# Kernel tuning notes

Hardware: AMD Instinct MI355X
Metric: run time of the kernel (lower is better)

## Reference

```python
import jax, jax.numpy as jnp
import numpy as np

NEG = -1000000.0

def setup_inputs() -> dict:
    key = jax.random.key(0)
    k1, k2, k3, k4 = jax.random.split(key, 4)
    B, S, D = 32, 2048, 64  # batch_eff=batch*heads, seq_len, head_dim
    queries = jax.random.normal(k1, (B, S, D), dtype=jnp.float32)
    keys = jax.random.normal(k2, (B, S, D), dtype=jnp.float32)
    values = jax.random.normal(k3, (B, S, D), dtype=jnp.float32)
    valid_len = jax.random.randint(k4, (B,), 1, S + 1, dtype=jnp.int32)
    return {"queries": queries, "keys": keys, "values": values, "valid_len": valid_len}

def reference(queries, keys, values, valid_len):
    # scores: (B, Sq, Sk) = QK^T / sqrt(d)
    d = queries.shape[-1]
    scores = jnp.einsum('bqd,bkd->bqk', queries, keys) / jnp.sqrt(jnp.float32(d))
    # padding mask from per-batch valid key lengths: True where position is padded
    k_len = keys.shape[1]
    pad_mask = jnp.arange(k_len)[None, None, :] >= valid_len[:, None, None]  # (B,1,Sk)
    scores = jnp.where(pad_mask, NEG, scores)
    attn = jax.nn.softmax(scores, axis=-1)
    # dropout is identity in eval / reference mode
    return jnp.einsum('bqk,bkd->bqd', attn, values)
```

## Files before the change

### kernel.cpp

```cpp
#include <hip/hip_runtime.h>

typedef unsigned short ushort_t;
typedef short short8 __attribute__((ext_vector_type(8)));
typedef float f32x4 __attribute__((ext_vector_type(4)));
typedef unsigned int u32x4 __attribute__((ext_vector_type(4)));

typedef f32x4 f32x4a __attribute__((may_alias));
typedef u32x4 u32x4a __attribute__((may_alias));
typedef short8 short8a __attribute__((may_alias));

#define BC 64
#define PRP 74

#define BAR_LGKM() asm volatile("s_waitcnt lgkmcnt(0)\n\ts_barrier" ::: "memory")
#define BAR_VM4()  asm volatile("s_waitcnt vmcnt(4)\n\ts_barrier" ::: "memory")
#define BAR_VM0()  asm volatile("s_waitcnt vmcnt(0)\n\ts_barrier" ::: "memory")

__device__ __forceinline__ ushort_t f2bf(float x) {
    unsigned u = __float_as_uint(x);
    u = (u + 0x7fffu + ((u >> 16) & 1u)) >> 16;
    return (ushort_t)u;
}

__device__ __forceinline__ void dma16(const void* g, void* lds) {
    __builtin_amdgcn_global_load_lds(
        (const __attribute__((address_space(1))) unsigned int*)g,
        (__attribute__((address_space(3))) unsigned int*)lds, 16, 0, 0);
}

__global__ __launch_bounds__(256) void prep_kv(
    const float* __restrict__ K, const float* __restrict__ V,
    ushort_t* __restrict__ Kb, ushort_t* __restrict__ Vt, int S, int jtiles)
{
    __shared__ ushort_t T[64 * 66];
    const int b  = blockIdx.x / jtiles;
    const int j0 = (blockIdx.x % jtiles) * 64;
    const int tid = threadIdx.x;

    {
        const int jj = tid >> 2, d0 = (tid & 3) * 16;
        const float* src = K + ((size_t)b * S + j0 + jj) * 64 + d0;
        f32x4 k0 = *(const f32x4a*)(src),     k1 = *(const f32x4a*)(src + 4);
        f32x4 k2 = *(const f32x4a*)(src + 8), k3 = *(const f32x4a*)(src + 12);
        u32x4 w0, w1;
#pragma unroll
        for (int k = 0; k < 2; ++k) {
            w0[k]   = (unsigned)f2bf(k0[2*k]) | ((unsigned)f2bf(k0[2*k+1]) << 16);
            w0[k+2] = (unsigned)f2bf(k1[2*k]) | ((unsigned)f2bf(k1[2*k+1]) << 16);
            w1[k]   = (unsigned)f2bf(k2[2*k]) | ((unsigned)f2bf(k2[2*k+1]) << 16);
            w1[k+2] = (unsigned)f2bf(k3[2*k]) | ((unsigned)f2bf(k3[2*k+1]) << 16);
        }
        ushort_t* dst = Kb + ((size_t)b * S + j0 + jj) * 64 + d0;
        *(u32x4a*)dst = w0;
        *(u32x4a*)(dst + 8) = w1;
    }

    {
        const float* Vb = V + ((size_t)b * S + j0) * 64;
#pragma unroll
        for (int p = 0; p < 4; ++p) {
            int jj = p * 16 + (tid >> 4), d4 = (tid & 15) * 4;
            f32x4 v = *(const f32x4a*)(Vb + (size_t)jj * 64 + d4);
#pragma unroll
            for (int k = 0; k < 4; ++k) T[(d4 + k) * 66 + jj] = f2bf(v[k]);
        }
        __syncthreads();
        const int d = tid >> 2, j16 = (tid & 3) * 16;
        ushort_t* dst = Vt + ((size_t)b * 64 + d) * S + j0 + j16;
        u32x4 w0, w1;
#pragma unroll
        for (int k = 0; k < 4; ++k) {
            w0[k] = (unsigned)T[d*66 + j16 + 2*k]     | ((unsigned)T[d*66 + j16 + 2*k + 1] << 16);
            w1[k] = (unsigned)T[d*66 + j16 + 8 + 2*k] | ((unsigned)T[d*66 + j16 + 9 + 2*k] << 16);
        }
        *(u32x4a*)dst = w0;
        *(u32x4a*)(dst + 8) = w1;
    }
}

__global__ __launch_bounds__(256, 3) void attn_persist(
    const float* __restrict__ Q, const ushort_t* __restrict__ Kb,
    const ushort_t* __restrict__ Vt, const int* __restrict__ VL,
    float* __restrict__ O, int* __restrict__ cnt,
    int NB, int S, int qtiles, int nitems)
{
    __shared__ __align__(16) ushort_t Kbuf[2][64 * 64];
    __shared__ __align__(16) ushort_t Vbuf[2][64 * 64];
    __shared__ ushort_t Psh[4 * 16 * PRP];
    __shared__ int order_s[64];
    __shared__ int item_s;

    const int tid  = threadIdx.x;
    const int wave = tid >> 6;
    const int lane = tid & 63;
    const int qd   = lane >> 4;
    const int c    = lane & 15;
    const int q8   = qd * 8;

    if (tid < NB && NB <= 64) {
        const int myL = VL[tid];
        int rank = 0;
        for (int j = 0; j < NB; ++j) {
            const int Lj = VL[j];
            rank += (Lj > myL) || (Lj == myL && j < tid);
        }
        order_s[rank] = tid;
    }
    __syncthreads();

    const int r0 = 8 * (wave * 2) + (lane >> 3);
    const int r1 = r0 + 8;
    const int bdp = lane & 7;
    const int swz0 = ((bdp - r0) & 7) * 16;
    const int swz1 = ((bdp - r1) & 7) * 16;
    const int ldsoff0 = (wave * 2) * 512;
    const int ldsoff1 = ldsoff0 + 512;

    int off[2][4];
#pragma unroll
    for (int x = 0; x < 2; ++x)
#pragma unroll
        for (int y = 0; y < 4; ++y) {
            const int row = y * 16 + c;
            off[x][y] = row * 128 + (((x * 4 + qd) + row) & 7) * 16;
        }

    const float qs = 0.125f * 1.4426950408889634f;
    const f32x4 zero4 = {0.0f, 0.0f, 0.0f, 0.0f};
    ushort_t* Pw = Psh + wave * (16 * PRP);

    for (;;) {
        if (tid == 0) item_s = atomicAdd(cnt, 1);
        __syncthreads();
        const int it = item_s;
        if (it >= nitems) break;

        const int b  = order_s[it / qtiles];
        const int qt = it % qtiles;
        const int qrow0 = qt * 64 + wave * 16;
        const int L   = VL[b];
        const int nkt = (L + BC - 1) / BC;

        short8 qf[2];
        {
            const float* Qb = Q + ((size_t)b * S + qrow0) * 64;
#pragma unroll
            for (int kc = 0; kc < 2; ++kc) {
                const float* p = Qb + c * 64 + kc * 32 + q8;
                f32x4 a = *(const f32x4a*)p;
                f32x4 bq = *(const f32x4a*)(p + 4);
                short8 f;
#pragma unroll
                for (int k = 0; k < 4; ++k) {
                    f[k]   = (short)f2bf(a[k] * qs);
                    f[k+4] = (short)f2bf(bq[k] * qs);
                }
                qf[kc] = f;
            }
        }

        f32x4 oacc[4];
#pragma unroll
        for (int dt = 0; dt < 4; ++dt) oacc[dt] = zero4;
        float lrow[4] = {0.0f, 0.0f, 0.0f, 0.0f};

        const char* KbB = (const char*)(Kb + (size_t)b * S * 64);
        const char* VtB = (const char*)(Vt + (size_t)b * 64 * S);
        const char* kg0 = KbB + r0 * 128 + swz0;
        const char* kg1 = KbB + r1 * 128 + swz1;
        const char* vg0 = VtB + (size_t)r0 * (S * 2) + swz0;
        const char* vg1 = VtB + (size_t)r1 * (S * 2) + swz1;

        dma16(kg0, Kbuf[0] + ldsoff0);
        dma16(kg1, Kbuf[0] + ldsoff1);
        dma16(vg0, Vbuf[0] + ldsoff0);
        dma16(vg1, Vbuf[0] + ldsoff1);

        for (int kt = 0; kt < nkt; ++kt) {
            const int j0 = kt * BC;
            const ushort_t* Kt  = Kbuf[kt & 1];
            const ushort_t* Vb_ = Vbuf[kt & 1];

            if (kt + 1 < nkt) {
                const size_t ko = (size_t)(kt + 1) * 8192;
                const size_t vo = (size_t)(kt + 1) * 128;
                ushort_t* kb = Kbuf[(kt + 1) & 1];
                ushort_t* vb = Vbuf[(kt + 1) & 1];
                dma16(kg0 + ko, kb + ldsoff0);
                dma16(kg1 + ko, kb + ldsoff1);
                dma16(vg0 + vo, vb + ldsoff0);
                dma16(vg1 + vo, vb + ldsoff1);
                BAR_VM4();
            } else {
                BAR_VM0();
            }

            f32x4 sacc[4];
#pragma unroll
            for (int nt = 0; nt < 4; ++nt) sacc[nt] = zero4;
#pragma unroll
            for (int kc = 0; kc < 2; ++kc) {
#pragma unroll
                for (int nt = 0; nt < 4; ++nt) {
                    short8 kf = *(const short8a*)((const char*)Kt + off[kc][nt]);
                    sacc[nt] = __builtin_amdgcn_mfma_f32_16x16x32_bf16(qf[kc], kf, sacc[nt], 0, 0, 0);
                }
            }

#pragma unroll
            for (int nt = 0; nt < 4; ++nt) {
                const bool valid = (j0 + nt * 16 + c) < L;
#pragma unroll
                for (int r = 0; r < 4; ++r) {
                    float p = valid ? exp2f(sacc[nt][r]) : 0.0f;
                    lrow[r] += p;
                    Pw[(qd * 4 + r) * PRP + nt * 16 + c] = f2bf(p);
                }
            }

#pragma unroll
            for (int jc = 0; jc < 2; ++jc) {
                short8 pf = *(const short8a*)&Pw[c * PRP + jc * 32 + q8];
#pragma unroll
                for (int dt = 0; dt < 4; ++dt) {
                    short8 vf = *(const short8a*)((const char*)Vb_ + off[jc][dt]);
                    oacc[dt] = __builtin_amdgcn_mfma_f32_16x16x32_bf16(pf, vf, oacc[dt], 0, 0, 0);
                }
            }

            BAR_LGKM();
        }

#pragma unroll
        for (int r = 0; r < 4; ++r) {
            float ls = lrow[r];
            ls += __shfl_xor(ls, 1);
            ls += __shfl_xor(ls, 2);
            ls += __shfl_xor(ls, 4);
            ls += __shfl_xor(ls, 8);
            const float inv = 1.0f / ls;
            const int row = qrow0 + qd * 4 + r;
            float* dst = O + ((size_t)b * S + row) * 64;
#pragma unroll
            for (int dt = 0; dt < 4; ++dt)
                dst[dt * 16 + c] = oacc[dt][r] * inv;
        }
    }
}

__global__ __launch_bounds__(256, 4) void attn_mono(
    const float* __restrict__ Q, const float* __restrict__ K,
    const float* __restrict__ V, const int* __restrict__ VL,
    float* __restrict__ O, int NB, int S)
{
    __shared__ ushort_t Ksh[BC * PRP];
    __shared__ ushort_t Vsh[64 * PRP];
    __shared__ ushort_t Psh[4 * 16 * PRP];
    const int tid = threadIdx.x, wave = tid >> 6, lane = tid & 63;
    const int qd = lane >> 4, c = lane & 15, q8 = qd * 8;
    const int bid = blockIdx.x;
    const int b = (bid & 7) | (((bid >> 3) & 3) << 3);
    const int qt = bid >> 5;
    const int qrow0 = qt * 64 + wave * 16;
    const int L = VL[b];
    const int nkt = (L + BC - 1) / BC;
    const size_t bbase = (size_t)b * S * 64;
    const int kj = tid >> 2, kd = (tid & 3) * 16;
    const int vp = tid & 31, vd = (tid >> 5) * 8;
    const float qs = 0.125f * 1.4426950408889634f;
    short8 qf[2];
    {
        const float* Qb = Q + bbase + (size_t)qrow0 * 64;
#pragma unroll
        for (int kc = 0; kc < 2; ++kc) {
            const float* p = Qb + c * 64 + kc * 32 + q8;
            f32x4 a = *(const f32x4a*)p;
            f32x4 bq = *(const f32x4a*)(p + 4);
            short8 f;
#pragma unroll
            for (int k = 0; k < 4; ++k) { f[k] = (short)f2bf(a[k]*qs); f[k+4] = (short)f2bf(bq[k]*qs); }
            qf[kc] = f;
        }
    }
    const f32x4 zero4 = {0.0f, 0.0f, 0.0f, 0.0f};
    f32x4 oacc[4];
#pragma unroll
    for (int dt = 0; dt < 4; ++dt) oacc[dt] = zero4;
    float lrow[4] = {0, 0, 0, 0};
    ushort_t* Pw = Psh + wave * (16 * PRP);
    for (int kt = 0; kt < nkt; ++kt) {
        const int j0 = kt * BC;
        __syncthreads();
        {
            const float* src = K + bbase + (size_t)(j0 + kj) * 64 + kd;
            f32x4 k0 = *(const f32x4a*)(src), k1 = *(const f32x4a*)(src + 4);
            f32x4 k2 = *(const f32x4a*)(src + 8), k3 = *(const f32x4a*)(src + 12);
            u32x4 w0, w1;
#pragma unroll
            for (int k = 0; k < 2; ++k) {
                w0[k]   = (unsigned)f2bf(k0[2*k]) | ((unsigned)f2bf(k0[2*k+1]) << 16);
                w0[k+2] = (unsigned)f2bf(k1[2*k]) | ((unsigned)f2bf(k1[2*k+1]) << 16);
                w1[k]   = (unsigned)f2bf(k2[2*k]) | ((unsigned)f2bf(k2[2*k+1]) << 16);
                w1[k+2] = (unsigned)f2bf(k3[2*k]) | ((unsigned)f2bf(k3[2*k+1]) << 16);
            }
            *(u32x4a*)&Ksh[kj * PRP + kd] = w0;
            *(u32x4a*)&Ksh[kj * PRP + kd + 8] = w1;
        }
        {
            const float* src = V + bbase + (size_t)(j0 + 2 * vp) * 64 + vd;
            f32x4 a0 = *(const f32x4a*)(src), a1 = *(const f32x4a*)(src + 4);
            f32x4 b0 = *(const f32x4a*)(src + 64), b1 = *(const f32x4a*)(src + 68);
#pragma unroll
            for (int kk = 0; kk < 8; ++kk) {
                float av = (kk < 4) ? a0[kk & 3] : a1[kk & 3];
                float bv = (kk < 4) ? b0[kk & 3] : b1[kk & 3];
                *(unsigned __attribute__((may_alias))*)&Vsh[(vd + kk) * PRP + 2 * vp] =
                    (unsigned)f2bf(av) | ((unsigned)f2bf(bv) << 16);
            }
        }
        __syncthreads();
        f32x4 sacc[4];
#pragma unroll
        for (int nt = 0; nt < 4; ++nt) sacc[nt] = zero4;
#pragma unroll
        for (int kc = 0; kc < 2; ++kc)
#pragma unroll
            for (int nt = 0; nt < 4; ++nt) {
                short8 kf = *(const short8a*)&Ksh[(nt * 16 + c) * PRP + kc * 32 + q8];
                sacc[nt] = __builtin_amdgcn_mfma_f32_16x16x32_bf16(qf[kc], kf, sacc[nt], 0, 0, 0);
            }
#pragma unroll
        for (int nt = 0; nt < 4; ++nt) {
            const bool valid = (j0 + nt * 16 + c) < L;
#pragma unroll
            for (int r = 0; r < 4; ++r) {
                float p = valid ? exp2f(sacc[nt][r]) : 0.0f;
                lrow[r] += p;
                Pw[(qd * 4 + r) * PRP + nt * 16 + c] = f2bf(p);
            }
        }
#pragma unroll
        for (int jc = 0; jc < 2; ++jc) {
            short8 pf = *(const short8a*)&Pw[c * PRP + jc * 32 + q8];
#pragma unroll
            for (int dt = 0; dt < 4; ++dt) {
                short8 vf = *(const short8a*)&Vsh[(dt * 16 + c) * PRP + jc * 32 + q8];
                oacc[dt] = __builtin_amdgcn_mfma_f32_16x16x32_bf16(pf, vf, oacc[dt], 0, 0, 0);
            }
        }
    }
#pragma unroll
    for (int r = 0; r < 4; ++r) {
        float ls = lrow[r];
        ls += __shfl_xor(ls, 1); ls += __shfl_xor(ls, 2);
        ls += __shfl_xor(ls, 4); ls += __shfl_xor(ls, 8);
        const float inv = 1.0f / ls;
        const int row = qrow0 + qd * 4 + r;
        float* dst = O + bbase + (size_t)row * 64;
#pragma unroll
        for (int dt = 0; dt < 4; ++dt) dst[dt * 16 + c] = oacc[dt][r] * inv;
    }
}

extern "C" void kernel_launch(void* const* d_in, const int* in_sizes, int n_in,
                              void* d_out, int out_size, void* d_ws, size_t ws_size,
                              hipStream_t stream) {
    const float* Q = (const float*)d_in[0];
    const float* K = (const float*)d_in[1];
    const float* V = (const float*)d_in[2];
    const int*  VL = (const int*)d_in[3];
    float*      Op = (float*)d_out;

    const int NB = in_sizes[3];
    const int S  = in_sizes[0] / (NB * 64);
    const int qtiles = S / 64;
    const int jtiles = S / 64;
    const size_t nelem = (size_t)NB * S * 64;
    const size_t bf_bytes = nelem * 2;

    if (ws_size >= 256 + 2 * bf_bytes && NB <= 64) {
        int* cnt = (int*)d_ws;
        ushort_t* Kb = (ushort_t*)((char*)d_ws + 256);
        ushort_t* Vt = (ushort_t*)((char*)d_ws + 256 + bf_bytes);
        hipMemsetAsync(d_ws, 0, 256, stream);
        prep_kv<<<dim3(NB * jtiles), dim3(256), 0, stream>>>(K, V, Kb, Vt, S, jtiles);
        const int nitems = NB * qtiles;
        attn_persist<<<dim3(768), dim3(256), 0, stream>>>(
            Q, Kb, Vt, VL, Op, cnt, NB, S, qtiles, nitems);
    } else {
        attn_mono<<<dim3(NB * qtiles), dim3(256), 0, stream>>>(Q, K, V, VL, Op, NB, S);
    }
}
```

Measured before the change: 173.1 us.

## Compute transposed QK^T so P stays in registers, dropping the LDS P round-trip

The QK^T MFMA swaps its operands so the score accumulator comes out transposed. The K rows are loaded into LDS in a permuted order so that each lane's exp values line up directly with the B-operand fragment of the PV MFMA. This removes the per-wave P shared-memory buffer along with its stores and reloads. The row-sum reduction now uses cross-quad shuffles plus a broadcast shuffle at the end. Occupancy rises to 4 blocks per CU and the persistent grid grows to 1024, at the risk of register pressure from the new launch bound.

```diff
diff --git a/kernel.cpp b/kernel.cpp
--- a/kernel.cpp
+++ b/kernel.cpp
@@ -78,7 +78,7 @@
     }
 }
 
-__global__ __launch_bounds__(256, 3) void attn_persist(
+__global__ __launch_bounds__(256, 4) void attn_persist(
     const float* __restrict__ Q, const ushort_t* __restrict__ Kb,
     const ushort_t* __restrict__ Vt, const int* __restrict__ VL,
     float* __restrict__ O, int* __restrict__ cnt,
@@ -86,7 +86,6 @@
 {
     __shared__ __align__(16) ushort_t Kbuf[2][64 * 64];
     __shared__ __align__(16) ushort_t Vbuf[2][64 * 64];
-    __shared__ ushort_t Psh[4 * 16 * PRP];
     __shared__ int order_s[64];
     __shared__ int item_s;
 
@@ -108,13 +107,16 @@
     }
     __syncthreads();
 
-    const int r0 = 8 * (wave * 2) + (lane >> 3);
+    const int r0 = wave * 16 + (lane >> 3);
     const int r1 = r0 + 8;
     const int bdp = lane & 7;
     const int swz0 = ((bdp - r0) & 7) * 16;
     const int swz1 = ((bdp - r1) & 7) * 16;
-    const int ldsoff0 = (wave * 2) * 512;
+    const int ldsoff0 = wave * 1024;
     const int ldsoff1 = ldsoff0 + 512;
+
+    const int pr0 = ((r0 >> 4) & 1) * 32 + ((r0 >> 2) & 3) * 8 + ((r0 >> 5) & 1) * 4 + (r0 & 3);
+    const int pr1 = ((r1 >> 4) & 1) * 32 + ((r1 >> 2) & 3) * 8 + ((r1 >> 5) & 1) * 4 + (r1 & 3);
 
     int off[2][4];
 #pragma unroll
@@ -127,7 +129,6 @@
 
     const float qs = 0.125f * 1.4426950408889634f;
     const f32x4 zero4 = {0.0f, 0.0f, 0.0f, 0.0f};
-    ushort_t* Pw = Psh + wave * (16 * PRP);
 
     for (;;) {
         if (tid == 0) item_s = atomicAdd(cnt, 1);
@@ -146,9 +147,9 @@
             const float* Qb = Q + ((size_t)b * S + qrow0) * 64;
 #pragma unroll
             for (int kc = 0; kc < 2; ++kc) {
-                const float* p = Qb + c * 64 + kc * 32 + q8;
-                f32x4 a = *(const f32x4a*)p;
-                f32x4 bq = *(const f32x4a*)(p + 4);
+                const float* qp = Qb + c * 64 + kc * 32 + q8;
+                f32x4 a = *(const f32x4a*)qp;
+                f32x4 bq = *(const f32x4a*)(qp + 4);
                 short8 f;
 #pragma unroll
                 for (int k = 0; k < 4; ++k) {
@@ -162,12 +163,12 @@
         f32x4 oacc[4];
 #pragma unroll
         for (int dt = 0; dt < 4; ++dt) oacc[dt] = zero4;
-        float lrow[4] = {0.0f, 0.0f, 0.0f, 0.0f};
+        float rs0 = 0.0f, rs1 = 0.0f;
 
         const char* KbB = (const char*)(Kb + (size_t)b * S * 64);
         const char* VtB = (const char*)(Vt + (size_t)b * 64 * S);
-        const char* kg0 = KbB + r0 * 128 + swz0;
-        const char* kg1 = KbB + r1 * 128 + swz1;
+        const char* kg0 = KbB + pr0 * 128 + swz0;
+        const char* kg1 = KbB + pr1 * 128 + swz1;
         const char* vg0 = VtB + (size_t)r0 * (S * 2) + swz0;
         const char* vg1 = VtB + (size_t)r1 * (S * 2) + swz1;
 
@@ -203,24 +204,32 @@
 #pragma unroll
                 for (int nt = 0; nt < 4; ++nt) {
                     short8 kf = *(const short8a*)((const char*)Kt + off[kc][nt]);
-                    sacc[nt] = __builtin_amdgcn_mfma_f32_16x16x32_bf16(qf[kc], kf, sacc[nt], 0, 0, 0);
+                    sacc[nt] = __builtin_amdgcn_mfma_f32_16x16x32_bf16(kf, qf[kc], sacc[nt], 0, 0, 0);
                 }
             }
 
+            const int lim = L - j0 - q8;
+            float p[4][4];
 #pragma unroll
             for (int nt = 0; nt < 4; ++nt) {
-                const bool valid = (j0 + nt * 16 + c) < L;
+                const int kb2 = (nt & 1) * 32 + ((nt >> 1) << 2);
 #pragma unroll
                 for (int r = 0; r < 4; ++r) {
-                    float p = valid ? exp2f(sacc[nt][r]) : 0.0f;
-                    lrow[r] += p;
-                    Pw[(qd * 4 + r) * PRP + nt * 16 + c] = f2bf(p);
+                    const bool valid = (kb2 + r < lim);
+                    const float e = valid ? exp2f(sacc[nt][r]) : 0.0f;
+                    p[nt][r] = e;
+                    if (nt & 1) rs1 += e; else rs0 += e;
                 }
             }
 
 #pragma unroll
             for (int jc = 0; jc < 2; ++jc) {
-                short8 pf = *(const short8a*)&Pw[c * PRP + jc * 32 + q8];
+                u32x4 w;
+                w[0] = (unsigned)f2bf(p[jc][0])     | ((unsigned)f2bf(p[jc][1])     << 16);
+                w[1] = (unsigned)f2bf(p[jc][2])     | ((unsigned)f2bf(p[jc][3])     << 16);
+                w[2] = (unsigned)f2bf(p[jc + 2][0]) | ((unsigned)f2bf(p[jc + 2][1]) << 16);
+                w[3] = (unsigned)f2bf(p[jc + 2][2]) | ((unsigned)f2bf(p[jc + 2][3]) << 16);
+                const short8 pf = __builtin_bit_cast(short8, w);
 #pragma unroll
                 for (int dt = 0; dt < 4; ++dt) {
                     short8 vf = *(const short8a*)((const char*)Vb_ + off[jc][dt]);
@@ -231,19 +240,18 @@
             BAR_LGKM();
         }
 
+        float rsum = rs0 + rs1;
+        rsum += __shfl_xor(rsum, 16);
+        rsum += __shfl_xor(rsum, 32);
+        const float inv = 1.0f / rsum;
 #pragma unroll
         for (int r = 0; r < 4; ++r) {
-            float ls = lrow[r];
-            ls += __shfl_xor(ls, 1);
-            ls += __shfl_xor(ls, 2);
-            ls += __shfl_xor(ls, 4);
-            ls += __shfl_xor(ls, 8);
-            const float inv = 1.0f / ls;
+            const float invr = __shfl(inv, (lane & 48) | (qd * 4 + r));
             const int row = qrow0 + qd * 4 + r;
             float* dst = O + ((size_t)b * S + row) * 64;
 #pragma unroll
             for (int dt = 0; dt < 4; ++dt)
-                dst[dt * 16 + c] = oacc[dt][r] * inv;
+                dst[dt * 16 + c] = oacc[dt][r] * invr;
         }
     }
 }
@@ -385,7 +393,8 @@
         hipMemsetAsync(d_ws, 0, 256, stream);
         prep_kv<<<dim3(NB * jtiles), dim3(256), 0, stream>>>(K, V, Kb, Vt, S, jtiles);
         const int nitems = NB * qtiles;
-        attn_persist<<<dim3(768), dim3(256), 0, stream>>>(
+        const int grid = nitems < 1024 ? nitems : 1024;
+        attn_persist<<<dim3(grid), dim3(256), 0, stream>>>(
             Q, Kb, Vt, VL, Op, cnt, NB, S, qtiles, nitems);
     } else {
         attn_mono<<<dim3(NB * qtiles), dim3(256), 0, stream>>>(Q, K, V, VL, Op, NB, S);
```

New measurement: 169.4 us. -2.1%, faster.
